# Performance work log

Measured on AMD Instinct MI355X. Metric: run time of the kernel, lower is better.

The kernel has to match this reference:

```python
import jax, jax.numpy as jnp
import numpy as np


def setup_inputs() -> dict:
    B, I, H = 4096, 512, 1024
    key = jax.random.key(0)
    ks = jax.random.split(key, 10)
    return {
        "input": jax.random.normal(ks[0], (B, I), dtype=jnp.float32),
        "t": jax.random.uniform(ks[1], (B, 1), dtype=jnp.float32),
        "hx": jax.random.normal(ks[2], (B, H), dtype=jnp.float32),
        "cx": jax.random.normal(ks[3], (B, H), dtype=jnp.float32),
        "weight_ih": jax.random.normal(ks[4], (4 * H, I), dtype=jnp.float32),
        "weight_hh": jax.random.normal(ks[5], (4 * H, H), dtype=jnp.float32),
        "bias_ih": jax.random.normal(ks[6], (4 * H,), dtype=jnp.float32),
        "bias_hh": jax.random.normal(ks[7], (4 * H,), dtype=jnp.float32),
        "W_decomp": jax.random.normal(ks[8], (H, H), dtype=jnp.float32),
        "b_decomp": jax.random.normal(ks[9], (H,), dtype=jnp.float32),
    }


def reference(input, t, hx, cx, weight_ih, weight_hh, bias_ih, bias_hh, W_decomp, b_decomp):
    H = W_decomp.shape[0]
    # gates: [B, 4H]
    gates = input @ weight_ih.T + bias_ih + hx @ weight_hh.T + bias_hh
    ingate, forgetgate, cellgate, outgate = jnp.split(gates, 4, axis=1)
    # time-decay factor g(t): elementwise 1/t where t != 0, broadcast [B,1] -> [B,H]
    T = jnp.where(t != 0, 1.0 / jnp.where(t != 0, t, 1.0), 0.0)  # [B, 1]
    T = jnp.broadcast_to(T, (t.shape[0], H))
    # T-LSTM cell-state decomposition
    C_ST = jnp.tanh(cx @ W_decomp + b_decomp)
    cx_adj = cx - C_ST + T * C_ST
    ingate = jax.nn.sigmoid(ingate)
    forgetgate = jax.nn.sigmoid(forgetgate)
    cellgate = jnp.tanh(cellgate)
    outgate = jax.nn.sigmoid(outgate)
    cy = forgetgate * cx_adj + ingate * cellgate
    hy = outgate * jnp.tanh(cy)
    return (hy, cy)
```

## Files before the change

kernel.cpp:

```cpp
#include <hip/hip_runtime.h>
#include <cstdint>


typedef __attribute__((ext_vector_type(8))) __bf16 bf16x8;
typedef __attribute__((ext_vector_type(16))) float f32x16;
typedef __attribute__((ext_vector_type(8))) unsigned short ushort8;

__device__ __forceinline__ unsigned short f2bf_rn(float f) {
  unsigned int u = __float_as_uint(f);
  unsigned int r = u + 0x7fffu + ((u >> 16) & 1u);
  return (unsigned short)(r >> 16);
}
__device__ __forceinline__ float bf2f(unsigned short h) {
  return __uint_as_float(((unsigned int)h) << 16);
}
__device__ __forceinline__ float sigm_f(float x) {
  return 1.0f / (1.0f + __expf(-x));
}
__device__ __forceinline__ float tanh_f(float x) {
  return 1.0f - 2.0f / (__expf(2.0f * x) + 1.0f);
}
__device__ __forceinline__ void gl_lds16(const void* g, void* l) {
  __builtin_amdgcn_global_load_lds(
      (const __attribute__((address_space(1))) void*)g,
      (__attribute__((address_space(3))) void*)l, 16, 0, 0);
}

__device__ __forceinline__ void cvt16(const float* __restrict__ s,
                                      unsigned short* __restrict__ hi,
                                      unsigned short* __restrict__ lo) {
  float4 v[4];
#pragma unroll
  for (int i = 0; i < 4; ++i) v[i] = ((const float4*)s)[i];
  const float* f = (const float*)v;
  ushort8 h[2], l[2];
#pragma unroll
  for (int i = 0; i < 16; ++i) {
    unsigned short hh = f2bf_rn(f[i]);
    ((unsigned short*)h)[i] = hh;
    ((unsigned short*)l)[i] = f2bf_rn(f[i] - bf2f(hh));
  }
  ((ushort8*)hi)[0] = h[0];
  ((ushort8*)hi)[1] = h[1];
  ((ushort8*)lo)[0] = l[0];
  ((ushort8*)lo)[1] = l[1];
}

__global__ __launch_bounds__(256) void prep_k(
    const float* __restrict__ input, const float* __restrict__ hx,
    const float* __restrict__ w_ih, const float* __restrict__ w_hh,
    const float* __restrict__ cx, const float* __restrict__ Wd,
    unsigned short* __restrict__ Xhi, unsigned short* __restrict__ Xlo,
    unsigned short* __restrict__ Whi, unsigned short* __restrict__ Wlo,
    unsigned short* __restrict__ Chi, unsigned short* __restrict__ Clo,
    unsigned short* __restrict__ Dhi, unsigned short* __restrict__ Dlo) {
  const int bid = blockIdx.x;
  const int tid = threadIdx.x;
  if (bid < 1536) {
    const int u = bid * 256 + tid;
    const int row = u / 96;
    const int col = (u % 96) << 4;
    const float* src = (col < 512) ? (input + (long)row * 512 + col)
                                   : (hx + (long)row * 1024 + (col - 512));
    cvt16(src, Xhi + (long)row * 1536 + col, Xlo + (long)row * 1536 + col);
  } else if (bid < 3072) {
    const int u = (bid - 1536) * 256 + tid;
    const int n = u / 96;
    const int col = (u % 96) << 4;
    const int g = n >> 10;
    const int h = n & 1023;
    const long nd = ((h >> 5) << 7) | (g << 5) | (h & 31);
    const float* src = (col < 512) ? (w_ih + (long)n * 512 + col)
                                   : (w_hh + (long)n * 1024 + (col - 512));
    cvt16(src, Whi + nd * 1536 + col, Wlo + nd * 1536 + col);
  } else if (bid < 4096) {
    const int u = (bid - 3072) * 256 + tid;
    const int row = u >> 6;
    const int col = (u & 63) << 4;
    cvt16(cx + (long)row * 1024 + col, Chi + (long)row * 1024 + col,
          Clo + (long)row * 1024 + col);
  } else {
    __shared__ float tile[64][65];
    const int bid2 = bid - 4096;
    const int bx = (bid2 & 15) * 64;
    const int by = (bid2 >> 4) * 64;
    const int tx = tid & 63;
    const int ty = tid >> 6;
    for (int r = ty; r < 64; r += 4)
      tile[r][tx] = Wd[(long)(by + r) * 1024 + bx + tx];
    __syncthreads();
    for (int r = ty; r < 64; r += 4) {
      float v = tile[tx][r];
      unsigned short h = f2bf_rn(v);
      long o = (long)(bx + r) * 1024 + by + tx;
      Dhi[o] = h;
      Dlo[o] = f2bf_rn(v - bf2f(h));
    }
  }
}

__global__ __launch_bounds__(256) void gemm_mega(
    const unsigned short* __restrict__ Xh, const unsigned short* __restrict__ Xl,
    const unsigned short* __restrict__ Wh, const unsigned short* __restrict__ Wl,
    const unsigned short* __restrict__ Ch, const unsigned short* __restrict__ Cl,
    const unsigned short* __restrict__ Dh, const unsigned short* __restrict__ Dl,
    const float* __restrict__ b_ih, const float* __restrict__ b_hh,
    const float* __restrict__ b_d, const float* __restrict__ cx,
    const float* __restrict__ t, float* __restrict__ out) {
  __shared__ __align__(16) unsigned short sBh[128 * 64];
  __shared__ __align__(16) unsigned short sBl[128 * 64];

  const int n_blk = blockIdx.x & 31;
  const int m_blk = blockIdx.x >> 5;
  const int m0 = m_blk * 128;
  const int n0 = n_blk * 128;
  const int h0 = n_blk * 32;

  const int tid = threadIdx.x;
  const int wave = tid >> 6;
  const int lane = tid & 63;
  const int lm = lane & 31;
  const int lk = lane >> 5;
  const int lmw = lm & 7;
  const int sg = lane >> 3;
  const int sq = (lane & 7) ^ sg;

  f32x16 dacc;
#pragma unroll
  for (int r = 0; r < 16; ++r) dacc[r] = 0.f;
  {
    const long arow = (long)(m0 + wave * 32 + lm) * 1024 + lk * 8;
    const long brow = (long)(h0 + wave * 8 + sg) * 1024 + sq * 8;
    unsigned short* dsth = sBh + (wave * 8) * 64;
    unsigned short* dstl = sBl + (wave * 8) * 64;
    for (int kt = 0; kt < 1024; kt += 64) {
      bf16x8 ah[4], al[4];
#pragma unroll
      for (int kh = 0; kh < 4; ++kh) {
        ah[kh] = *(const bf16x8*)(Ch + arow + kt + kh * 16);
        al[kh] = *(const bf16x8*)(Cl + arow + kt + kh * 16);
      }
      gl_lds16(Dh + brow + kt, dsth);
      gl_lds16(Dl + brow + kt, dstl);
      __syncthreads();
#pragma unroll
      for (int kh = 0; kh < 4; ++kh) {
        const int pc = ((kh * 2 + lk) ^ lmw) << 3;
        bf16x8 bh = *(const bf16x8*)(sBh + lm * 64 + pc);
        bf16x8 bl = *(const bf16x8*)(sBl + lm * 64 + pc);
        dacc = __builtin_amdgcn_mfma_f32_32x32x16_bf16(ah[kh], bh, dacc, 0, 0, 0);
        dacc = __builtin_amdgcn_mfma_f32_32x32x16_bf16(ah[kh], bl, dacc, 0, 0, 0);
        dacc = __builtin_amdgcn_mfma_f32_32x32x16_bf16(al[kh], bh, dacc, 0, 0, 0);
      }
      __syncthreads();
    }
  }

  f32x16 acc[4];
#pragma unroll
  for (int j = 0; j < 4; ++j)
#pragma unroll
    for (int r = 0; r < 16; ++r) acc[j][r] = 0.f;
  {
    const long arow = (long)(m0 + wave * 32 + lm) * 1536 + lk * 8;
    const long brow = (long)(n0 + wave * 32 + sg) * 1536 + sq * 8;
    for (int kt = 0; kt < 1536; kt += 64) {
      bf16x8 ah[4], al[4];
#pragma unroll
      for (int kh = 0; kh < 4; ++kh) {
        ah[kh] = *(const bf16x8*)(Xh + arow + kt + kh * 16);
        al[kh] = *(const bf16x8*)(Xl + arow + kt + kh * 16);
      }
#pragma unroll
      for (int i = 0; i < 4; ++i) {
        const long gb = brow + (long)i * 8 * 1536 + kt;
        const int loff = (wave * 32 + i * 8) * 64;
        gl_lds16(Wh + gb, sBh + loff);
        gl_lds16(Wl + gb, sBl + loff);
      }
      __syncthreads();
#pragma unroll
      for (int kh = 0; kh < 4; ++kh) {
        const int pc = ((kh * 2 + lk) ^ lmw) << 3;
        bf16x8 bh[4], bl[4];
#pragma unroll
        for (int nb = 0; nb < 4; ++nb) {
          bh[nb] = *(const bf16x8*)(sBh + (nb * 32 + lm) * 64 + pc);
          bl[nb] = *(const bf16x8*)(sBl + (nb * 32 + lm) * 64 + pc);
        }
#pragma unroll
        for (int nb = 0; nb < 4; ++nb) {
          acc[nb] = __builtin_amdgcn_mfma_f32_32x32x16_bf16(ah[kh], bh[nb], acc[nb], 0, 0, 0);
          acc[nb] = __builtin_amdgcn_mfma_f32_32x32x16_bf16(ah[kh], bl[nb], acc[nb], 0, 0, 0);
          acc[nb] = __builtin_amdgcn_mfma_f32_32x32x16_bf16(al[kh], bh[nb], acc[nb], 0, 0, 0);
        }
      }
      __syncthreads();
    }
  }

  const int h = h0 + lm;
  const float bsum_i = b_ih[h] + b_hh[h];
  const float bsum_f = b_ih[1024 + h] + b_hh[1024 + h];
  const float bsum_g = b_ih[2048 + h] + b_hh[2048 + h];
  const float bsum_o = b_ih[3072 + h] + b_hh[3072 + h];
  const float bd = b_d[h];
#pragma unroll
  for (int reg = 0; reg < 16; ++reg) {
    const int m = m0 + wave * 32 + (reg & 3) + 8 * (reg >> 2) + 4 * lk;
    const float tv = t[m];
    const float T = (tv != 0.0f) ? (1.0f / tv) : 0.0f;
    const float cst = tanh_f(dacc[reg] + bd);
    const float cadj = cx[(long)m * 1024 + h] + (T - 1.0f) * cst;
    const float ig = sigm_f(acc[0][reg] + bsum_i);
    const float fg = sigm_f(acc[1][reg] + bsum_f);
    const float cg = tanh_f(acc[2][reg] + bsum_g);
    const float og = sigm_f(acc[3][reg] + bsum_o);
    const float cy = fg * cadj + ig * cg;
    const float hy = og * tanh_f(cy);
    out[(long)m * 1024 + h] = hy;
    out[4096L * 1024 + (long)m * 1024 + h] = cy;
  }
}

extern "C" void kernel_launch(void* const* d_in, const int* in_sizes, int n_in,
                              void* d_out, int out_size, void* d_ws, size_t ws_size,
                              hipStream_t stream) {
  const float* input = (const float*)d_in[0];
  const float* t     = (const float*)d_in[1];
  const float* hx    = (const float*)d_in[2];
  const float* cx    = (const float*)d_in[3];
  const float* w_ih  = (const float*)d_in[4];
  const float* w_hh  = (const float*)d_in[5];
  const float* b_ih  = (const float*)d_in[6];
  const float* b_hh  = (const float*)d_in[7];
  const float* Wd    = (const float*)d_in[8];
  const float* b_d   = (const float*)d_in[9];

  const long B = 4096, H = 1024, KX = 1536, NG = 4096;

  char* ws = (char*)d_ws;
  unsigned short* Xhi = (unsigned short*)ws; ws += B * KX * 2;
  unsigned short* Xlo = (unsigned short*)ws; ws += B * KX * 2;
  unsigned short* Whi = (unsigned short*)ws; ws += NG * KX * 2;
  unsigned short* Wlo = (unsigned short*)ws; ws += NG * KX * 2;
  unsigned short* Chi = (unsigned short*)ws; ws += B * H * 2;
  unsigned short* Clo = (unsigned short*)ws; ws += B * H * 2;
  unsigned short* Dhi = (unsigned short*)ws; ws += H * H * 2;
  unsigned short* Dlo = (unsigned short*)ws; ws += H * H * 2;

  prep_k<<<4352, 256, 0, stream>>>(input, hx, w_ih, w_hh, cx, Wd,
                                   Xhi, Xlo, Whi, Wlo, Chi, Clo, Dhi, Dlo);
  gemm_mega<<<1024, 256, 0, stream>>>(Xhi, Xlo, Whi, Wlo, Chi, Clo, Dhi, Dlo,
                                      b_ih, b_hh, b_d, cx, t, (float*)d_out);
}
```

Measured before the change: 361.3 us.

## Stage A operand in LDS and switch to 16x16x32 MFMA tiles

Both GEMM phases now stage the A operand (hi/lo bf16 splits of X and cx) into LDS with global_load_lds, alongside B. Previously each wave loaded A directly from global into registers. The MFMA shape moves from 32x32x16 to 16x16x32, with each wave holding a 2x8 grid of 16x16 accumulators and a new XOR swizzle for LDS reads. The aim is to cut per-wave global traffic and use the newer MFMA shape, at the cost of more LDS traffic and more LDS reads per MFMA. The LDS buffers are laid out as two K-halves rather than double-buffered, so there is no overlap of loads with compute.

Result: faster. 335.7 us (-7.1%).

```diff
diff --git a/kernel.cpp b/kernel.cpp
--- a/kernel.cpp
+++ b/kernel.cpp
@@ -3,7 +3,7 @@
 
 
 typedef __attribute__((ext_vector_type(8))) __bf16 bf16x8;
-typedef __attribute__((ext_vector_type(16))) float f32x16;
+typedef __attribute__((ext_vector_type(4))) float f32x4;
 typedef __attribute__((ext_vector_type(8))) unsigned short ushort8;
 
 __device__ __forceinline__ unsigned short f2bf_rn(float f) {
@@ -107,8 +107,10 @@
     const float* __restrict__ b_ih, const float* __restrict__ b_hh,
     const float* __restrict__ b_d, const float* __restrict__ cx,
     const float* __restrict__ t, float* __restrict__ out) {
-  __shared__ __align__(16) unsigned short sBh[128 * 64];
-  __shared__ __align__(16) unsigned short sBl[128 * 64];
+  __shared__ __align__(16) unsigned short sAh[2][128 * 32];
+  __shared__ __align__(16) unsigned short sAl[2][128 * 32];
+  __shared__ __align__(16) unsigned short sBh[2][128 * 32];
+  __shared__ __align__(16) unsigned short sBl[2][128 * 32];
 
   const int n_blk = blockIdx.x & 31;
   const int m_blk = blockIdx.x >> 5;
@@ -119,107 +121,140 @@
   const int tid = threadIdx.x;
   const int wave = tid >> 6;
   const int lane = tid & 63;
-  const int lm = lane & 31;
-  const int lk = lane >> 5;
-  const int lmw = lm & 7;
-  const int sg = lane >> 3;
-  const int sq = (lane & 7) ^ sg;
-
-  f32x16 dacc;
-#pragma unroll
-  for (int r = 0; r < 16; ++r) dacc[r] = 0.f;
+  const int srow = lane >> 2;
+  const int ssw = (((lane & 3) ^ ((lane >> 3) & 3)) << 3);
+  const int fm = lane & 15;
+  const int fq = lane >> 4;
+  const int psw = (fq ^ ((fm >> 1) & 3)) << 3;
+
+  f32x4 dacc[2][2];
+#pragma unroll
+  for (int i = 0; i < 2; ++i)
+#pragma unroll
+    for (int j = 0; j < 2; ++j) dacc[i][j] = {0.f, 0.f, 0.f, 0.f};
+
   {
-    const long arow = (long)(m0 + wave * 32 + lm) * 1024 + lk * 8;
-    const long brow = (long)(h0 + wave * 8 + sg) * 1024 + sq * 8;
-    unsigned short* dsth = sBh + (wave * 8) * 64;
-    unsigned short* dstl = sBl + (wave * 8) * 64;
+    const unsigned short* dsrc = (wave < 2) ? Dh : Dl;
+    const int drow = (wave & 1) * 16;
+    const long dgbase = (long)(h0 + drow + srow) * 1024 + ssw;
     for (int kt = 0; kt < 1024; kt += 64) {
-      bf16x8 ah[4], al[4];
-#pragma unroll
-      for (int kh = 0; kh < 4; ++kh) {
-        ah[kh] = *(const bf16x8*)(Ch + arow + kt + kh * 16);
-        al[kh] = *(const bf16x8*)(Cl + arow + kt + kh * 16);
-      }
-      gl_lds16(Dh + brow + kt, dsth);
-      gl_lds16(Dl + brow + kt, dstl);
+#pragma unroll
+      for (int s = 0; s < 2; ++s) {
+#pragma unroll
+        for (int r = 0; r < 2; ++r) {
+          const int rowb = r * 64 + wave * 16;
+          const long gA = (long)(m0 + rowb + srow) * 1024 + kt + s * 32 + ssw;
+          gl_lds16(Ch + gA, sAh[s] + rowb * 32);
+          gl_lds16(Cl + gA, sAl[s] + rowb * 32);
+        }
+        unsigned short* ddst = ((wave < 2) ? sBh[s] : sBl[s]) + drow * 32;
+        gl_lds16(dsrc + dgbase + kt + s * 32, ddst);
+      }
       __syncthreads();
 #pragma unroll
-      for (int kh = 0; kh < 4; ++kh) {
-        const int pc = ((kh * 2 + lk) ^ lmw) << 3;
-        bf16x8 bh = *(const bf16x8*)(sBh + lm * 64 + pc);
-        bf16x8 bl = *(const bf16x8*)(sBl + lm * 64 + pc);
-        dacc = __builtin_amdgcn_mfma_f32_32x32x16_bf16(ah[kh], bh, dacc, 0, 0, 0);
-        dacc = __builtin_amdgcn_mfma_f32_32x32x16_bf16(ah[kh], bl, dacc, 0, 0, 0);
-        dacc = __builtin_amdgcn_mfma_f32_32x32x16_bf16(al[kh], bh, dacc, 0, 0, 0);
+      for (int s = 0; s < 2; ++s) {
+        bf16x8 ah[2], al[2], bh[2], bl[2];
+#pragma unroll
+        for (int i = 0; i < 2; ++i) {
+          const int ao = (wave * 32 + i * 16 + fm) * 32 + psw;
+          ah[i] = *(const bf16x8*)(sAh[s] + ao);
+          al[i] = *(const bf16x8*)(sAl[s] + ao);
+          const int bo = (i * 16 + fm) * 32 + psw;
+          bh[i] = *(const bf16x8*)(sBh[s] + bo);
+          bl[i] = *(const bf16x8*)(sBl[s] + bo);
+        }
+#pragma unroll
+        for (int i = 0; i < 2; ++i)
+#pragma unroll
+          for (int j = 0; j < 2; ++j) {
+            dacc[i][j] = __builtin_amdgcn_mfma_f32_16x16x32_bf16(ah[i], bh[j], dacc[i][j], 0, 0, 0);
+            dacc[i][j] = __builtin_amdgcn_mfma_f32_16x16x32_bf16(ah[i], bl[j], dacc[i][j], 0, 0, 0);
+            dacc[i][j] = __builtin_amdgcn_mfma_f32_16x16x32_bf16(al[i], bh[j], dacc[i][j], 0, 0, 0);
+          }
       }
       __syncthreads();
     }
   }
 
-  f32x16 acc[4];
-#pragma unroll
-  for (int j = 0; j < 4; ++j)
-#pragma unroll
-    for (int r = 0; r < 16; ++r) acc[j][r] = 0.f;
-  {
-    const long arow = (long)(m0 + wave * 32 + lm) * 1536 + lk * 8;
-    const long brow = (long)(n0 + wave * 32 + sg) * 1536 + sq * 8;
-    for (int kt = 0; kt < 1536; kt += 64) {
-      bf16x8 ah[4], al[4];
-#pragma unroll
-      for (int kh = 0; kh < 4; ++kh) {
-        ah[kh] = *(const bf16x8*)(Xh + arow + kt + kh * 16);
-        al[kh] = *(const bf16x8*)(Xl + arow + kt + kh * 16);
-      }
-#pragma unroll
-      for (int i = 0; i < 4; ++i) {
-        const long gb = brow + (long)i * 8 * 1536 + kt;
-        const int loff = (wave * 32 + i * 8) * 64;
-        gl_lds16(Wh + gb, sBh + loff);
-        gl_lds16(Wl + gb, sBl + loff);
-      }
-      __syncthreads();
-#pragma unroll
-      for (int kh = 0; kh < 4; ++kh) {
-        const int pc = ((kh * 2 + lk) ^ lmw) << 3;
+  f32x4 acc[2][8];
+#pragma unroll
+  for (int i = 0; i < 2; ++i)
+#pragma unroll
+    for (int j = 0; j < 8; ++j) acc[i][j] = {0.f, 0.f, 0.f, 0.f};
+
+  for (int kt = 0; kt < 1536; kt += 64) {
+#pragma unroll
+    for (int s = 0; s < 2; ++s)
+#pragma unroll
+      for (int r = 0; r < 2; ++r) {
+        const int rowb = r * 64 + wave * 16;
+        const long gA = (long)(m0 + rowb + srow) * 1536 + kt + s * 32 + ssw;
+        const long gB = (long)(n0 + rowb + srow) * 1536 + kt + s * 32 + ssw;
+        gl_lds16(Xh + gA, sAh[s] + rowb * 32);
+        gl_lds16(Xl + gA, sAl[s] + rowb * 32);
+        gl_lds16(Wh + gB, sBh[s] + rowb * 32);
+        gl_lds16(Wl + gB, sBl[s] + rowb * 32);
+      }
+    __syncthreads();
+#pragma unroll
+    for (int s = 0; s < 2; ++s) {
+      bf16x8 ah[2], al[2];
+#pragma unroll
+      for (int i = 0; i < 2; ++i) {
+        const int ao = (wave * 32 + i * 16 + fm) * 32 + psw;
+        ah[i] = *(const bf16x8*)(sAh[s] + ao);
+        al[i] = *(const bf16x8*)(sAl[s] + ao);
+      }
+#pragma unroll
+      for (int jh = 0; jh < 2; ++jh) {
         bf16x8 bh[4], bl[4];
 #pragma unroll
-        for (int nb = 0; nb < 4; ++nb) {
-          bh[nb] = *(const bf16x8*)(sBh + (nb * 32 + lm) * 64 + pc);
-          bl[nb] = *(const bf16x8*)(sBl + (nb * 32 + lm) * 64 + pc);
+        for (int jj = 0; jj < 4; ++jj) {
+          const int bo = ((jh * 4 + jj) * 16 + fm) * 32 + psw;
+          bh[jj] = *(const bf16x8*)(sBh[s] + bo);
+          bl[jj] = *(const bf16x8*)(sBl[s] + bo);
         }
 #pragma unroll
-        for (int nb = 0; nb < 4; ++nb) {
-          acc[nb] = __builtin_amdgcn_mfma_f32_32x32x16_bf16(ah[kh], bh[nb], acc[nb], 0, 0, 0);
-          acc[nb] = __builtin_amdgcn_mfma_f32_32x32x16_bf16(ah[kh], bl[nb], acc[nb], 0, 0, 0);
-          acc[nb] = __builtin_amdgcn_mfma_f32_32x32x16_bf16(al[kh], bh[nb], acc[nb], 0, 0, 0);
-        }
-      }
-      __syncthreads();
-    }
-  }
-
-  const int h = h0 + lm;
-  const float bsum_i = b_ih[h] + b_hh[h];
-  const float bsum_f = b_ih[1024 + h] + b_hh[1024 + h];
-  const float bsum_g = b_ih[2048 + h] + b_hh[2048 + h];
-  const float bsum_o = b_ih[3072 + h] + b_hh[3072 + h];
-  const float bd = b_d[h];
-#pragma unroll
-  for (int reg = 0; reg < 16; ++reg) {
-    const int m = m0 + wave * 32 + (reg & 3) + 8 * (reg >> 2) + 4 * lk;
-    const float tv = t[m];
-    const float T = (tv != 0.0f) ? (1.0f / tv) : 0.0f;
-    const float cst = tanh_f(dacc[reg] + bd);
-    const float cadj = cx[(long)m * 1024 + h] + (T - 1.0f) * cst;
-    const float ig = sigm_f(acc[0][reg] + bsum_i);
-    const float fg = sigm_f(acc[1][reg] + bsum_f);
-    const float cg = tanh_f(acc[2][reg] + bsum_g);
-    const float og = sigm_f(acc[3][reg] + bsum_o);
-    const float cy = fg * cadj + ig * cg;
-    const float hy = og * tanh_f(cy);
-    out[(long)m * 1024 + h] = hy;
-    out[4096L * 1024 + (long)m * 1024 + h] = cy;
+        for (int i = 0; i < 2; ++i)
+#pragma unroll
+          for (int jj = 0; jj < 4; ++jj) {
+            const int j = jh * 4 + jj;
+            acc[i][j] = __builtin_amdgcn_mfma_f32_16x16x32_bf16(ah[i], bh[jj], acc[i][j], 0, 0, 0);
+            acc[i][j] = __builtin_amdgcn_mfma_f32_16x16x32_bf16(ah[i], bl[jj], acc[i][j], 0, 0, 0);
+            acc[i][j] = __builtin_amdgcn_mfma_f32_16x16x32_bf16(al[i], bh[jj], acc[i][j], 0, 0, 0);
+          }
+      }
+    }
+    __syncthreads();
+  }
+
+#pragma unroll
+  for (int j0 = 0; j0 < 2; ++j0) {
+    const int h = h0 + j0 * 16 + fm;
+    const float bsum_i = b_ih[h] + b_hh[h];
+    const float bsum_f = b_ih[1024 + h] + b_hh[1024 + h];
+    const float bsum_g = b_ih[2048 + h] + b_hh[2048 + h];
+    const float bsum_o = b_ih[3072 + h] + b_hh[3072 + h];
+    const float bd = b_d[h];
+#pragma unroll
+    for (int i = 0; i < 2; ++i) {
+#pragma unroll
+      for (int r = 0; r < 4; ++r) {
+        const int m = m0 + wave * 32 + i * 16 + fq * 4 + r;
+        const float tv = t[m];
+        const float T = (tv != 0.0f) ? (1.0f / tv) : 0.0f;
+        const float cst = tanh_f(dacc[i][j0][r] + bd);
+        const float cadj = cx[(long)m * 1024 + h] + (T - 1.0f) * cst;
+        const float ig = sigm_f(acc[i][0 + j0][r] + bsum_i);
+        const float fg = sigm_f(acc[i][2 + j0][r] + bsum_f);
+        const float cg = tanh_f(acc[i][4 + j0][r] + bsum_g);
+        const float og = sigm_f(acc[i][6 + j0][r] + bsum_o);
+        const float cy = fg * cadj + ig * cg;
+        const float hy = og * tanh_f(cy);
+        out[(long)m * 1024 + h] = hy;
+        out[4096L * 1024 + (long)m * 1024 + h] = cy;
+      }
+    }
   }
 }
 
```
